# Kernel optimization log

Hardware: AMD Instinct MI355X
Metric: run time of the kernel (lower is better)

## Reference

```python
import jax, jax.numpy as jnp
import numpy as np

B, C, H, W = 32, 64, 128, 128

def setup_inputs() -> dict:
    key = jax.random.key(0)
    k1, k2, k3, k4 = jax.random.split(key, 4)
    x = jax.random.normal(k1, (B, C, H, W), dtype=jnp.float32)
    theta = jax.random.normal(k2, (C, C), dtype=jnp.float32) * (6.0 / (C + C)) ** 0.5  # xavier-ish
    W_lin = jax.random.normal(k3, (C, C), dtype=jnp.float32) * (1.0 / C) ** 0.5
    b_lin = jax.random.normal(k4, (C,), dtype=jnp.float32) * 0.01
    return {"x": x, "theta": theta, "W_lin": W_lin, "b_lin": b_lin}

def reference(x, theta, W_lin, b_lin):
    b, c, h, w = x.shape
    # channel descriptor: global average pool -> [B, C]
    wvec = jnp.mean(x, axis=(2, 3))
    # pairwise diff and soft adjacency, batched over B
    diff = wvec[:, :, None] - wvec[:, None, :]              # [B, C, C]
    e = jnp.exp(-diff)
    T = jnp.abs(1.0 - e / (1.0 + e)) - 1.0                  # [B, C, C]
    A = 0.5 * (T + jnp.swapaxes(T, 1, 2)) * theta           # [B, C, C]
    # graph conv: A @ x_flat, relu
    x_flat = x.reshape(b, c, h * w)                         # [B, C, HW]
    Hmat = jax.nn.relu(jnp.einsum('bij,bjn->bin', A, x_flat))  # [B, C, HW]
    # Linear over channel dim applied to H.T: [B, HW, C]
    Hout = jnp.einsum('bin,ci->bnc', Hmat, W_lin) + b_lin   # [B, HW, C]
    # faithful to torch: H.view(C, h, w) is a raw row-major reshape of [HW, C]
    return Hout.reshape(b, c, h, w)
```

## Files before the change

kernel.cpp:

```cpp
#include <hip/hip_runtime.h>

static constexpr int Cc  = 64;
static constexpr int HWc = 16384;
static constexpr int Bc  = 32;
static constexpr int PXB = 1024;
static constexpr int PH  = 64;
static constexpr int NPH = PXB / PH;


typedef _Float16 v8h __attribute__((ext_vector_type(8)));
typedef float    v4f __attribute__((ext_vector_type(4)));

union FragU { uint32_t u[4]; v8h h; };

__device__ inline uint32_t packf2(float lo, float hi) {
  union { _Float16 h[2]; uint32_t u; } r;
  r.h[0] = (_Float16)lo; r.h[1] = (_Float16)hi;
  return r.u;
}

__device__ inline v4f mfma16(v8h a, v8h b, v4f c) {
  return __builtin_amdgcn_mfma_f32_16x16x32_f16(a, b, c, 0, 0, 0);
}

__device__ inline void gload_lds4(const float* g, float* l) {
  __builtin_amdgcn_global_load_lds(
      (const __attribute__((address_space(1))) void*)g,
      (__attribute__((address_space(3))) void*)l, 4, 0, 0);
}

__global__ void prep_weights(const float* __restrict__ theta,
                             const float* __restrict__ Wlin,
                             _Float16* __restrict__ M1h,
                             _Float16* __restrict__ Wh) {
  int t = blockIdx.x * 256 + threadIdx.x;
  if (t < Cc * Cc) {
    M1h[t] = (_Float16)(-0.5f * theta[t]);
    Wh[t]  = (_Float16)(Wlin[t]);
  }
}

__global__ __launch_bounds__(256) void fused_mfma(
    const float* __restrict__ x,
    const _Float16* __restrict__ M1h,
    const _Float16* __restrict__ Wh,
    const float* __restrict__ blin,
    float* __restrict__ out)
{
  __shared__ __align__(16) float    xbuf[2][64][65];
  __shared__ __align__(16) _Float16 M1l[64][72];
  __shared__ __align__(16) _Float16 Wl [64][72];
  __shared__ __align__(16) _Float16 p2 [4][16][72];

  const int tid  = threadIdx.x;
  const int wv   = tid >> 6;
  const int l    = tid & 63;
  const int lq   = tid & 15;
  const int quad = l >> 4;
  const int pxw  = wv * 16 + lq;

  const int b   = blockIdx.x >> 4;
  const int px0 = (blockIdx.x & 15) * PXB;
  const float* xb = x + (size_t)b * Cc * HWc;

  {
    const int r = tid >> 2, seg = (tid & 3) * 16;
    const uint4 m0 = *(const uint4*)(M1h + r * 64 + seg);
    const uint4 m1 = *(const uint4*)(M1h + r * 64 + seg + 8);
    const uint4 w0 = *(const uint4*)(Wh  + r * 64 + seg);
    const uint4 w1 = *(const uint4*)(Wh  + r * 64 + seg + 8);
    *(uint4*)&M1l[r][seg]     = m0;
    *(uint4*)&M1l[r][seg + 8] = m1;
    *(uint4*)&Wl[r][seg]      = w0;
    *(uint4*)&Wl[r][seg + 8]  = w1;
  }
  v4f bias4[4];
#pragma unroll
  for (int ct = 0; ct < 4; ++ct)
    bias4[ct] = *(const v4f*)(blin + ct * 16 + quad * 4);

#pragma unroll
  for (int i = 0; i < 16; ++i) {
    const int c = wv * 16 + i;
    gload_lds4(xb + (size_t)c * HWc + px0 + l, &xbuf[0][c][0]);
  }

  __syncthreads();

  for (int t = 0; t < NPH; ++t) {
    if (t < NPH - 1) {
      const int pb = px0 + (t + 1) * PH;
      float* dst = &xbuf[(t + 1) & 1][0][0];
#pragma unroll
      for (int i = 0; i < 16; ++i) {
        const int c = wv * 16 + i;
        gload_lds4(xb + (size_t)c * HWc + pb + l, dst + c * 65);
      }
      __builtin_amdgcn_sched_barrier(0);
    }

    const int kb = t & 1;
    FragU xf[2];
#pragma unroll
    for (int kt = 0; kt < 2; ++kt)
#pragma unroll
      for (int r = 0; r < 4; ++r) {
        const int c0 = kt * 32 + quad * 8 + 2 * r;
        xf[kt].u[r] = packf2(xbuf[kb][c0][pxw], xbuf[kb][c0 + 1][pxw]);
      }

#pragma unroll
    for (int it = 0; it < 4; ++it) {
      v4f a = {0.f, 0.f, 0.f, 0.f};
#pragma unroll
      for (int kt = 0; kt < 2; ++kt)
        a = mfma16(*(const v8h*)&M1l[it * 16 + lq][kt * 32 + quad * 8],
                   xf[kt].h, a);
      uint2 w;
      w.x = packf2(fmaxf(a[0], 0.f), fmaxf(a[1], 0.f));
      w.y = packf2(fmaxf(a[2], 0.f), fmaxf(a[3], 0.f));
      *(uint2*)&p2[wv][lq][it * 16 + quad * 4] = w;
    }

    FragU pr[2];
#pragma unroll
    for (int kt = 0; kt < 2; ++kt)
      pr[kt].h = *(const v8h*)&p2[wv][lq][kt * 32 + quad * 8];

    float* orow = out + ((size_t)b * HWc + px0 + t * PH + pxw) * Cc + quad * 4;
#pragma unroll
    for (int ct = 0; ct < 4; ++ct) {
      v4f a = bias4[ct];
#pragma unroll
      for (int kt = 0; kt < 2; ++kt)
        a = mfma16(*(const v8h*)&Wl[ct * 16 + lq][kt * 32 + quad * 8],
                   pr[kt].h, a);
      *(v4f*)(orow + ct * 16) = a;
    }

    if (t < NPH - 1) {
      asm volatile("s_waitcnt vmcnt(4)" ::: "memory");
      __builtin_amdgcn_sched_barrier(0);
      __builtin_amdgcn_s_barrier();
      __builtin_amdgcn_sched_barrier(0);
    }
  }
}

extern "C" void kernel_launch(void* const* d_in, const int* in_sizes, int n_in,
                              void* d_out, int out_size, void* d_ws, size_t ws_size,
                              hipStream_t stream) {
  const float* x     = (const float*)d_in[0];
  const float* theta = (const float*)d_in[1];
  const float* W_lin = (const float*)d_in[2];
  const float* b_lin = (const float*)d_in[3];
  float* out = (float*)d_out;

  _Float16* M1h = (_Float16*)d_ws;
  _Float16* Wh  = M1h + Cc * Cc;

  prep_weights<<<(Cc * Cc + 255) / 256, 256, 0, stream>>>(theta, W_lin, M1h, Wh);

  const int nblocks = Bc * HWc / PXB;
  fused_mfma<<<nblocks, 256, 0, stream>>>(x, M1h, Wh, b_lin, out);
}
```

Measured before the change: 258.8 us.

## Register-prefetch x as float4, pack to fp16 pairs in LDS, hold weights in registers

Replaces the per-dword global-to-LDS loads with float4 register prefetches covering 256 pixels per phase. The prefetched values are packed into fp16 channel pairs before the LDS store, so the MFMA fragments are read directly without conversion. Weight fragments move from LDS into registers, and launch bounds ask for two blocks per CU. This cuts LDS traffic and load instruction count per byte, at the cost of higher register pressure and a longer gap between issuing a prefetch and consuming it.

```diff
diff --git a/kernel.cpp b/kernel.cpp
--- a/kernel.cpp
+++ b/kernel.cpp
@@ -4,7 +4,7 @@
 static constexpr int HWc = 16384;
 static constexpr int Bc  = 32;
 static constexpr int PXB = 1024;
-static constexpr int PH  = 64;
+static constexpr int PH  = 256;
 static constexpr int NPH = PXB / PH;
 
 
@@ -23,12 +23,6 @@
   return __builtin_amdgcn_mfma_f32_16x16x32_f16(a, b, c, 0, 0, 0);
 }
 
-__device__ inline void gload_lds4(const float* g, float* l) {
-  __builtin_amdgcn_global_load_lds(
-      (const __attribute__((address_space(1))) void*)g,
-      (__attribute__((address_space(3))) void*)l, 4, 0, 0);
-}
-
 __global__ void prep_weights(const float* __restrict__ theta,
                              const float* __restrict__ Wlin,
                              _Float16* __restrict__ M1h,
@@ -40,107 +34,119 @@
   }
 }
 
-__global__ __launch_bounds__(256) void fused_mfma(
+__global__ __launch_bounds__(256, 2) void fused_mfma(
     const float* __restrict__ x,
     const _Float16* __restrict__ M1h,
     const _Float16* __restrict__ Wh,
     const float* __restrict__ blin,
     float* __restrict__ out)
 {
-  __shared__ __align__(16) float    xbuf[2][64][65];
-  __shared__ __align__(16) _Float16 M1l[64][72];
-  __shared__ __align__(16) _Float16 Wl [64][72];
-  __shared__ __align__(16) _Float16 p2 [4][16][72];
+  __shared__ __align__(16) uint32_t xbuf[2][32][260];
+  __shared__ __align__(16) _Float16 p2[4][16][72];
 
   const int tid  = threadIdx.x;
   const int wv   = tid >> 6;
   const int l    = tid & 63;
   const int lq   = tid & 15;
   const int quad = l >> 4;
-  const int pxw  = wv * 16 + lq;
 
   const int b   = blockIdx.x >> 4;
   const int px0 = (blockIdx.x & 15) * PXB;
   const float* xb = x + (size_t)b * Cc * HWc;
 
-  {
-    const int r = tid >> 2, seg = (tid & 3) * 16;
-    const uint4 m0 = *(const uint4*)(M1h + r * 64 + seg);
-    const uint4 m1 = *(const uint4*)(M1h + r * 64 + seg + 8);
-    const uint4 w0 = *(const uint4*)(Wh  + r * 64 + seg);
-    const uint4 w1 = *(const uint4*)(Wh  + r * 64 + seg + 8);
-    *(uint4*)&M1l[r][seg]     = m0;
-    *(uint4*)&M1l[r][seg + 8] = m1;
-    *(uint4*)&Wl[r][seg]      = w0;
-    *(uint4*)&Wl[r][seg + 8]  = w1;
-  }
+  const v8h* M1v = (const v8h*)M1h;
+  const v8h* Whv = (const v8h*)Wh;
+  v8h w1[4][2], w2[4][2];
+#pragma unroll
+  for (int it = 0; it < 4; ++it)
+#pragma unroll
+    for (int kt = 0; kt < 2; ++kt) {
+      w1[it][kt] = M1v[(it * 16 + lq) * 8 + kt * 4 + quad];
+      w2[it][kt] = Whv[(it * 16 + lq) * 8 + kt * 4 + quad];
+    }
   v4f bias4[4];
 #pragma unroll
   for (int ct = 0; ct < 4; ++ct)
     bias4[ct] = *(const v4f*)(blin + ct * 16 + quad * 4);
 
+  {
+    float4 pe[8], po[8];
 #pragma unroll
-  for (int i = 0; i < 16; ++i) {
-    const int c = wv * 16 + i;
-    gload_lds4(xb + (size_t)c * HWc + px0 + l, &xbuf[0][c][0]);
+    for (int i = 0; i < 8; ++i) {
+      const int p = wv * 8 + i;
+      pe[i] = *(const float4*)(xb + (size_t)(2 * p)     * HWc + px0 + 4 * l);
+      po[i] = *(const float4*)(xb + (size_t)(2 * p + 1) * HWc + px0 + 4 * l);
+    }
+#pragma unroll
+    for (int i = 0; i < 8; ++i) {
+      uint4 w;
+      w.x = packf2(pe[i].x, po[i].x); w.y = packf2(pe[i].y, po[i].y);
+      w.z = packf2(pe[i].z, po[i].z); w.w = packf2(pe[i].w, po[i].w);
+      *(uint4*)&xbuf[0][wv * 8 + i][4 * l] = w;
+    }
   }
-
   __syncthreads();
 
   for (int t = 0; t < NPH; ++t) {
+    const int kb = t & 1;
+
+    float4 pe[8], po[8];
     if (t < NPH - 1) {
       const int pb = px0 + (t + 1) * PH;
-      float* dst = &xbuf[(t + 1) & 1][0][0];
 #pragma unroll
-      for (int i = 0; i < 16; ++i) {
-        const int c = wv * 16 + i;
-        gload_lds4(xb + (size_t)c * HWc + pb + l, dst + c * 65);
+      for (int i = 0; i < 8; ++i) {
+        const int p = wv * 8 + i;
+        pe[i] = *(const float4*)(xb + (size_t)(2 * p)     * HWc + pb + 4 * l);
+        po[i] = *(const float4*)(xb + (size_t)(2 * p + 1) * HWc + pb + 4 * l);
       }
       __builtin_amdgcn_sched_barrier(0);
     }
 
-    const int kb = t & 1;
-    FragU xf[2];
+    const int nb = wv * 64;
 #pragma unroll
-    for (int kt = 0; kt < 2; ++kt)
+    for (int nt = 0; nt < 4; ++nt) {
+      FragU xf[2];
 #pragma unroll
-      for (int r = 0; r < 4; ++r) {
-        const int c0 = kt * 32 + quad * 8 + 2 * r;
-        xf[kt].u[r] = packf2(xbuf[kb][c0][pxw], xbuf[kb][c0 + 1][pxw]);
+      for (int kt = 0; kt < 2; ++kt)
+#pragma unroll
+        for (int r = 0; r < 4; ++r)
+          xf[kt].u[r] = xbuf[kb][kt * 16 + quad * 4 + r][nb + nt * 16 + lq];
+
+#pragma unroll
+      for (int it = 0; it < 4; ++it) {
+        v4f a = {0.f, 0.f, 0.f, 0.f};
+        a = mfma16(w1[it][0], xf[0].h, a);
+        a = mfma16(w1[it][1], xf[1].h, a);
+        uint2 w;
+        w.x = packf2(fmaxf(a[0], 0.f), fmaxf(a[1], 0.f));
+        w.y = packf2(fmaxf(a[2], 0.f), fmaxf(a[3], 0.f));
+        *(uint2*)&p2[wv][lq][it * 16 + quad * 4] = w;
       }
 
+      FragU pr[2];
+      pr[0].h = *(const v8h*)&p2[wv][lq][quad * 8];
+      pr[1].h = *(const v8h*)&p2[wv][lq][32 + quad * 8];
+
+      float* orow = out + ((size_t)b * HWc + px0 + t * PH + nb + nt * 16 + lq) * Cc
+                    + quad * 4;
 #pragma unroll
-    for (int it = 0; it < 4; ++it) {
-      v4f a = {0.f, 0.f, 0.f, 0.f};
-#pragma unroll
-      for (int kt = 0; kt < 2; ++kt)
-        a = mfma16(*(const v8h*)&M1l[it * 16 + lq][kt * 32 + quad * 8],
-                   xf[kt].h, a);
-      uint2 w;
-      w.x = packf2(fmaxf(a[0], 0.f), fmaxf(a[1], 0.f));
-      w.y = packf2(fmaxf(a[2], 0.f), fmaxf(a[3], 0.f));
-      *(uint2*)&p2[wv][lq][it * 16 + quad * 4] = w;
-    }
-
-    FragU pr[2];
-#pragma unroll
-    for (int kt = 0; kt < 2; ++kt)
-      pr[kt].h = *(const v8h*)&p2[wv][lq][kt * 32 + quad * 8];
-
-    float* orow = out + ((size_t)b * HWc + px0 + t * PH + pxw) * Cc + quad * 4;
-#pragma unroll
-    for (int ct = 0; ct < 4; ++ct) {
-      v4f a = bias4[ct];
-#pragma unroll
-      for (int kt = 0; kt < 2; ++kt)
-        a = mfma16(*(const v8h*)&Wl[ct * 16 + lq][kt * 32 + quad * 8],
-                   pr[kt].h, a);
-      *(v4f*)(orow + ct * 16) = a;
+      for (int ct = 0; ct < 4; ++ct) {
+        v4f a = bias4[ct];
+        a = mfma16(w2[ct][0], pr[0].h, a);
+        a = mfma16(w2[ct][1], pr[1].h, a);
+        *(v4f*)(orow + ct * 16) = a;
+      }
     }
 
     if (t < NPH - 1) {
-      asm volatile("s_waitcnt vmcnt(4)" ::: "memory");
-      __builtin_amdgcn_sched_barrier(0);
+#pragma unroll
+      for (int i = 0; i < 8; ++i) {
+        uint4 w;
+        w.x = packf2(pe[i].x, po[i].x); w.y = packf2(pe[i].y, po[i].y);
+        w.z = packf2(pe[i].z, po[i].z); w.w = packf2(pe[i].w, po[i].w);
+        *(uint4*)&xbuf[kb ^ 1][wv * 8 + i][4 * l] = w;
+      }
+      asm volatile("s_waitcnt lgkmcnt(0)" ::: "memory");
       __builtin_amdgcn_s_barrier();
       __builtin_amdgcn_sched_barrier(0);
     }
```

Measured after the change: 251.8 us. 1.03x faster.
